# Optimization experiments

Hardware: AMD Instinct MI355X
Metric: run time of the kernel (lower is better)

The kernel has to match this reference:

```python
import jax, jax.numpy as jnp
import numpy as np

N_ITER = 3

def setup_inputs() -> dict:
    key = jax.random.key(0)
    k1, k2 = jax.random.split(key)
    x = jax.random.normal(k1, (8, 1024, 512), dtype=jnp.float32)
    W = jax.random.normal(k2, (4, 512, 512), dtype=jnp.float32)
    return {"x": x, "W": W}

def reference(x, W):
    # x: [B, N, D], W: [H, D, D]
    B, N, D = x.shape
    H = W.shape[0]
    scale = D ** (-0.5)
    logits = jnp.zeros((B, H, N, N), dtype=x.dtype)
    rw = None
    for _ in range(N_ITER):
        rw = jax.nn.softmax(logits, axis=-1)              # [B, H, N, N]
        # per-head bilinear scores: (x @ W_h) @ x^T * scale, batched over heads
        logits = jnp.einsum('bnd,hde,bme->bhnm', x, W, x) * scale
    # routing_weights @ x, then mean over heads -> [B, N, D]
    out = jnp.einsum('bhnm,bmd->bhnd', rw, x)
    return jnp.mean(out, axis=1)
```

## Files before the change

kernel.cpp:

```cpp
#include <hip/hip_runtime.h>
#include <math.h>

#define B_ 8
#define N_ 1024
#define D_ 512
#define H_ 4
#define ND (N_ * D_)
#define DD (D_ * D_)
#define NN (N_ * N_)

typedef _Float16 f16;
typedef f16 f16x8 __attribute__((ext_vector_type(8)));
typedef float f32x4 __attribute__((ext_vector_type(4)));

typedef __attribute__((address_space(3))) void lds_void;
typedef __attribute__((address_space(1))) void g_void;


#define MFMA8(QR, QC, AV, BV, IB)                                             \
    _Pragma("unroll")                                                         \
    for (int i_ = 0; i_ < 2; ++i_) {                                          \
        const int ii_ = (IB) + i_;                                            \
        _Pragma("unroll")                                                     \
        for (int j_ = 0; j_ < 2; ++j_) {                                      \
            acc[(QR)*4+ii_][(QC)*2+j_] = __builtin_amdgcn_mfma_f32_16x16x32_f16(AV[ii_][0], BV[j_][0], acc[(QR)*4+ii_][(QC)*2+j_], 0, 0, 0); \
            acc[(QR)*4+ii_][(QC)*2+j_] = __builtin_amdgcn_mfma_f32_16x16x32_f16(AV[ii_][1], BV[j_][1], acc[(QR)*4+ii_][(QC)*2+j_], 0, 0, 0); \
        }                                                                     \
    }

#define READ_A(AV, PA, HALF)                                                  \
    _Pragma("unroll")                                                         \
    for (int i_ = 0; i_ < 4; ++i_) {                                          \
        const int ra_ = (HALF) * 128 + wr * 64 + i_ * 16 + fr;                \
        AV[i_][0] = *(const f16x8*)(PA + ra_ * 64 + sw0 * 8);                 \
        AV[i_][1] = *(const f16x8*)(PA + ra_ * 64 + sw1 * 8);                 \
    }

#define READ_B(BV, PB, HALF)                                                  \
    _Pragma("unroll")                                                         \
    for (int j_ = 0; j_ < 2; ++j_) {                                          \
        const int rb_ = (HALF) * 128 + wc * 32 + j_ * 16 + fr;                \
        BV[j_][0] = *(const f16x8*)(PB + rb_ * 64 + sw0 * 8);                 \
        BV[j_][1] = *(const f16x8*)(PB + rb_ * 64 + sw1 * 8);                 \
    }

#define PHASE_RA(QR, QC, AV, BV, READS, STAGE, TAIL)                          \
    __builtin_amdgcn_s_barrier();                                             \
    asm volatile("s_waitcnt lgkmcnt(0)" ::: "memory");                        \
    __builtin_amdgcn_sched_barrier(0);                                        \
    __builtin_amdgcn_s_setprio(1);                                            \
    MFMA8(QR, QC, AV, BV, 0);                                                 \
    __builtin_amdgcn_s_setprio(0);                                            \
    __builtin_amdgcn_sched_barrier(0);                                        \
    READS;                                                                    \
    __builtin_amdgcn_sched_barrier(0);                                        \
    STAGE;                                                                    \
    __builtin_amdgcn_s_setprio(1);                                            \
    MFMA8(QR, QC, AV, BV, 2);                                                 \
    __builtin_amdgcn_s_setprio(0);                                            \
    TAIL;

template<int LDA, int LDB, int LDC, int KTOT>
__device__ __forceinline__ void gemm256(
    const f16* __restrict__ A, const f16* __restrict__ B,
    f16* __restrict__ C, float scale, int m0, int n0)
{
    constexpr int NT = KTOT / 64;
    static_assert(NT >= 2 && (NT % 2) == 0, "NT must be even");
    __shared__ f16 sA0[256 * 64];
    __shared__ f16 sB0[256 * 64];
    __shared__ f16 sA1[256 * 64];
    __shared__ f16 sB1[256 * 64];

    const int t = threadIdx.x;
    const int w = t >> 6, l = t & 63;
    const int fr = l & 15, fq = l >> 4;
    const int wr = w >> 2, wc = w & 3;
    const int lr = l >> 3, lc = l & 7;
    const int swc = lc ^ lr;
    const int sw0 = fq ^ (fr & 7);
    const int sw1 = (4 + fq) ^ (fr & 7);

    f32x4 acc[8][4] = {};

    auto stageA = [&](f16* buf, int half, int kt) {
#pragma unroll
        for (int i = 0; i < 2; ++i) {
            const int r0 = half * 128 + i * 64 + w * 8;
            const f16* g = A + (size_t)(m0 + r0 + lr) * LDA + kt * 64 + swc * 8;
            __builtin_amdgcn_global_load_lds((g_void*)g, (lds_void*)(buf + r0 * 64), 16, 0, 0);
        }
    };
    auto stageB = [&](f16* buf, int half, int kt) {
#pragma unroll
        for (int i = 0; i < 2; ++i) {
            const int r0 = half * 128 + i * 64 + w * 8;
            const f16* g = B + (size_t)(n0 + r0 + lr) * LDB + kt * 64 + swc * 8;
            __builtin_amdgcn_global_load_lds((g_void*)g, (lds_void*)(buf + r0 * 64), 16, 0, 0);
        }
    };

    stageA(sA0, 0, 0); stageB(sB0, 0, 0);
    stageA(sA0, 1, 0); stageB(sB0, 1, 0);
    stageA(sA1, 0, 1); stageB(sB1, 0, 1);
    asm volatile("s_waitcnt vmcnt(4)" ::: "memory");
    __builtin_amdgcn_s_barrier();

    f16x8 X[4][2], Y[4][2], U[2][2], V[2][2];
    READ_A(X, sA0, 0);
    READ_B(U, sB0, 0);

#define TAILCNT(KT)                                                           \
    { if ((KT) + 2 < NT) { asm volatile("s_waitcnt vmcnt(4)" ::: "memory"); } \
      else               { asm volatile("s_waitcnt vmcnt(0)" ::: "memory"); } }

#pragma unroll
    for (int tt = 0; tt < NT / 2; ++tt) {
        const int te = 2 * tt, to = 2 * tt + 1;
        PHASE_RA(0, 0, X, U, { READ_B(V, sB0, 1); },
                 { if (te + 1 < NT) stageA(sA1, 1, te + 1); }, {});
        PHASE_RA(0, 1, X, V, { READ_A(Y, sA0, 1); },
                 { if (te + 1 < NT) stageB(sB1, 1, te + 1); }, {});
        PHASE_RA(1, 1, Y, V, {},
                 { if (te + 2 < NT) stageA(sA0, 0, te + 2); }, {});
        PHASE_RA(1, 0, Y, U,
                 { if (te + 1 < NT) { READ_A(X, sA1, 0); READ_B(V, sB1, 0); } },
                 { if (te + 2 < NT) stageB(sB0, 0, te + 2); }, TAILCNT(te));
        PHASE_RA(0, 0, X, V, { READ_B(U, sB1, 1); },
                 { if (to + 1 < NT) stageA(sA0, 1, to + 1); }, {});
        PHASE_RA(0, 1, X, U, { READ_A(Y, sA1, 1); },
                 { if (to + 1 < NT) stageB(sB0, 1, to + 1); }, {});
        PHASE_RA(1, 1, Y, U, {},
                 { if (to + 2 < NT) stageA(sA1, 0, to + 2); }, {});
        PHASE_RA(1, 0, Y, V,
                 { if (to + 1 < NT) { READ_A(X, sA0, 0); READ_B(U, sB0, 0); } },
                 { if (to + 2 < NT) stageB(sB1, 0, to + 2); }, TAILCNT(to));
    }
#undef TAILCNT

#pragma unroll
    for (int ri = 0; ri < 8; ++ri)
#pragma unroll
        for (int cj = 0; cj < 4; ++cj)
#pragma unroll
            for (int rr = 0; rr < 4; ++rr) {
                const int row = m0 + (ri >> 2) * 128 + wr * 64 + (ri & 3) * 16 + fq * 4 + rr;
                const int col = n0 + (cj >> 1) * 128 + wc * 32 + (cj & 1) * 16 + fr;
                C[(size_t)row * LDC + col] = (f16)(acc[ri][cj][rr] * scale);
            }
}

template<int LDA, int LDB, int LDC, int KTOT>
__device__ __forceinline__ void single_core_f32(
    const f16* __restrict__ A, const f16* __restrict__ B0,
    float* __restrict__ C, int n0, int c0)
{
    __shared__ f16 sA[128 * 32];
    __shared__ f16 sB0[128 * 32];

    const int t = threadIdx.x;
    const int w = t >> 6;
    const int l = t & 63;
    const int lrow = l >> 2;
    const int lch  = l & 3;
    const int wr = w >> 1, wc = w & 1;
    const int fr = l & 15;
    const int fq = l >> 4;

    f32x4 acc[4][4] = {};

    for (int k0 = 0; k0 < KTOT; k0 += 32) {
#pragma unroll
        for (int i = 0; i < 2; ++i) {
            const int rb  = w * 2 + i;
            const int row = rb * 16 + lrow;
            const f16* ga = A + (size_t)(n0 + row) * LDA + k0 + lch * 8;
            __builtin_amdgcn_global_load_lds((g_void*)ga, (lds_void*)(sA + rb * 512), 16, 0, 0);
            const f16* gb0 = B0 + (size_t)(c0 + row) * LDB + k0 + lch * 8;
            __builtin_amdgcn_global_load_lds((g_void*)gb0, (lds_void*)(sB0 + rb * 512), 16, 0, 0);
        }
        __syncthreads();

        f16x8 a[4], b0[4];
#pragma unroll
        for (int i = 0; i < 4; ++i) {
            a[i]  = *(const f16x8*)(sA  + (wr * 64 + i * 16 + fr) * 32 + fq * 8);
            b0[i] = *(const f16x8*)(sB0 + (wc * 64 + i * 16 + fr) * 32 + fq * 8);
        }

#pragma unroll
        for (int i = 0; i < 4; ++i)
#pragma unroll
            for (int j = 0; j < 4; ++j)
                acc[i][j] = __builtin_amdgcn_mfma_f32_16x16x32_f16(a[i], b0[j], acc[i][j], 0, 0, 0);
        __syncthreads();
    }

#pragma unroll
    for (int i = 0; i < 4; ++i)
#pragma unroll
        for (int j = 0; j < 4; ++j)
#pragma unroll
            for (int r = 0; r < 4; ++r) {
                const int row = n0 + wr * 64 + i * 16 + fq * 4 + r;
                const int col = c0 + wc * 64 + j * 16 + fr;
                C[(size_t)row * LDC + col] = acc[i][j][r];
            }
}

__global__ __launch_bounds__(512, 2) void k_g1(
    const f16* __restrict__ xfh, const f16* __restrict__ wTh,
    f16* __restrict__ Yh)
{
    const int i = blockIdx.x;
    const int b = i & 7;
    const int li = i >> 3;
    const int h = li >> 3;
    const int tile = li & 7;
    const int m0 = (tile >> 1) * 256;
    const int n0 = (tile & 1) * 256;
    const int z = b * 4 + h;
    gemm256<D_, D_, D_, D_>(
        xfh + (size_t)b * ND,
        wTh + (size_t)h * DD,
        Yh + (size_t)z * ND, 1.0f, m0, n0);
}

__global__ __launch_bounds__(512, 2) void k_g2(
    const f16* __restrict__ Yh, const f16* __restrict__ xfh,
    f16* __restrict__ S)
{
    const int i = blockIdx.x;
    const int b = i & 7;
    const int li = i >> 3;
    const int h = li >> 4;
    const int tile = li & 15;
    const int m0 = (tile >> 2) * 256;
    const int n0 = (tile & 3) * 256;
    const int z = b * 4 + h;
    gemm256<D_, D_, N_, D_>(
        Yh + (size_t)z * ND,
        xfh + (size_t)b * ND,
        S + (size_t)z * NN, 0.044194173824159216f, m0, n0);
}

__global__ __launch_bounds__(256) void softmax_mean(
    const f16* __restrict__ S, f16* __restrict__ Pb)
{
    const int wave = threadIdx.x >> 6;
    const int l = threadIdx.x & 63;
    const int i = blockIdx.x;
    const int b = i & 7;
    const int rg = i >> 3;
    const int row = rg * 4 + wave;

    float o[16];
#pragma unroll
    for (int k = 0; k < 16; ++k) o[k] = 0.f;

#pragma unroll
    for (int h = 0; h < 4; ++h) {
        const f16x8* p = (const f16x8*)(S + ((size_t)(b * 4 + h) * N_ + row) * N_);
        f16x8 v0 = p[l * 2], v1 = p[l * 2 + 1];
        float f[16];
#pragma unroll
        for (int k = 0; k < 8; ++k) { f[k] = (float)v0[k]; f[k + 8] = (float)v1[k]; }
        float m = f[0];
#pragma unroll
        for (int k = 1; k < 16; ++k) m = fmaxf(m, f[k]);
#pragma unroll
        for (int off = 32; off > 0; off >>= 1) m = fmaxf(m, __shfl_xor(m, off));
        float s = 0.f;
#pragma unroll
        for (int k = 0; k < 16; ++k) { f[k] = __expf(f[k] - m); s += f[k]; }
#pragma unroll
        for (int off = 32; off > 0; off >>= 1) s += __shfl_xor(s, off);
        const float q = 0.25f / s;
#pragma unroll
        for (int k = 0; k < 16; ++k) o[k] += f[k] * q;
    }

    f16x8 o0, o1;
#pragma unroll
    for (int k = 0; k < 8; ++k) { o0[k] = (f16)o[k]; o1[k] = (f16)o[k + 8]; }
    f16x8* qp = (f16x8*)(Pb + ((size_t)b * N_ + row) * N_);
    qp[l * 2] = o0;
    qp[l * 2 + 1] = o1;
}

__global__ __launch_bounds__(256, 2) void k_g4b(
    const f16* __restrict__ Pb, const f16* __restrict__ xT,
    float* __restrict__ out)
{
    const int i = blockIdx.x;
    const int b = i & 7;
    const int li = i >> 3;
    const int m0 = (li >> 2) * 128;
    const int d0 = (li & 3) * 128;
    single_core_f32<N_, N_, D_, N_>(
        Pb + (size_t)b * NN,
        xT + (size_t)b * ND,
        out + (size_t)b * ND, m0, d0);
}

__global__ __launch_bounds__(256) void decomp_xw(
    const float* __restrict__ x, const float* __restrict__ W,
    f16* __restrict__ xfh, f16* __restrict__ xT, f16* __restrict__ wTh)
{
    __shared__ f16 tile[64][65];
    __shared__ float tw[64][65];
    const int t = threadIdx.x;
    const int z = blockIdx.z;
    if (z < 8) {
        const int b = z, n0 = blockIdx.y * 64, d0 = blockIdx.x * 64;
        const float* xb = x + (size_t)b * ND;
#pragma unroll
        for (int p = 0; p < 16; ++p) {
            const int idx = t + p * 256;
            const int r = idx >> 6, c = idx & 63;
            const float v = xb[(size_t)(n0 + r) * D_ + d0 + c];
            const f16 h = (f16)v;
            xfh[(size_t)b * ND + (size_t)(n0 + r) * D_ + d0 + c] = h;
            tile[r][c] = h;
        }
        __syncthreads();
#pragma unroll
        for (int p = 0; p < 16; ++p) {
            const int idx = t + p * 256;
            const int r = idx >> 6, c = idx & 63;
            xT[(size_t)b * ND + (size_t)(d0 + r) * N_ + n0 + c] = tile[c][r];
        }
    } else {
        if (blockIdx.y >= 8) return;
        const int h = z - 8, d0 = blockIdx.y * 64, e0 = blockIdx.x * 64;
        const float* Wh = W + (size_t)h * DD;
#pragma unroll
        for (int p = 0; p < 16; ++p) {
            const int idx = t + p * 256;
            const int r = idx >> 6, c = idx & 63;
            tw[r][c] = Wh[(size_t)(d0 + r) * D_ + e0 + c];
        }
        __syncthreads();
#pragma unroll
        for (int p = 0; p < 16; ++p) {
            const int idx = t + p * 256;
            const int r = idx >> 6, c = idx & 63;
            wTh[(size_t)h * DD + (size_t)(e0 + r) * D_ + d0 + c] = (f16)tw[c][r];
        }
    }
}

extern "C" void kernel_launch(void* const* d_in, const int* in_sizes, int n_in,
                              void* d_out, int out_size, void* d_ws, size_t ws_size,
                              hipStream_t stream) {
    const float* x = (const float*)d_in[0];
    const float* W = (const float*)d_in[1];
    float* out = (float*)d_out;

    char* ws = (char*)d_ws;
    const size_t MB = 1024 * 1024;
    f16*   xfh = (f16*)(ws + 0 * MB);
    f16*   xT  = (f16*)(ws + 8 * MB);
    f16*   wTh = (f16*)(ws + 16 * MB);
    f16*   Yh  = (f16*)(ws + 20 * MB);
    f16*   S   = (f16*)(ws + 52 * MB);
    f16*   Pb  = (f16*)(ws + 116 * MB);

    decomp_xw<<<dim3(8, 16, 12), 256, 0, stream>>>(x, W, xfh, xT, wTh);

    k_g1<<<dim3(256), 512, 0, stream>>>(xfh, wTh, Yh);
    k_g2<<<dim3(512), 512, 0, stream>>>(Yh, xfh, S);
    softmax_mean<<<dim3(2048), 256, 0, stream>>>(S, Pb);
    k_g4b<<<dim3(256), 256, 0, stream>>>(Pb, xT, out);
}
```

Before: 169.6 us.

## Vectorize transpose kernel, batch softmax loads, split score GEMM launch

```diff
diff --git a/kernel.cpp b/kernel.cpp
--- a/kernel.cpp
+++ b/kernel.cpp
@@ -10,6 +10,7 @@
 #define NN (N_ * N_)
 
 typedef _Float16 f16;
+typedef f16 f16x4 __attribute__((ext_vector_type(4)));
 typedef f16 f16x8 __attribute__((ext_vector_type(8)));
 typedef float f32x4 __attribute__((ext_vector_type(4)));
 
@@ -228,11 +229,11 @@
 
 __global__ __launch_bounds__(512, 2) void k_g2(
     const f16* __restrict__ Yh, const f16* __restrict__ xfh,
-    f16* __restrict__ S)
+    f16* __restrict__ S, int libase)
 {
     const int i = blockIdx.x;
     const int b = i & 7;
-    const int li = i >> 3;
+    const int li = (i >> 3) + libase * 32;
     const int h = li >> 4;
     const int tile = li & 15;
     const int m0 = (tile >> 2) * 256;
@@ -254,17 +255,23 @@
     const int rg = i >> 3;
     const int row = rg * 4 + wave;
 
-    float o[16];
-#pragma unroll
-    for (int k = 0; k < 16; ++k) o[k] = 0.f;
-
+    f16x8 va[4][2];
 #pragma unroll
     for (int h = 0; h < 4; ++h) {
         const f16x8* p = (const f16x8*)(S + ((size_t)(b * 4 + h) * N_ + row) * N_);
-        f16x8 v0 = p[l * 2], v1 = p[l * 2 + 1];
+        va[h][0] = p[l * 2];
+        va[h][1] = p[l * 2 + 1];
+    }
+
+    float o[16];
+#pragma unroll
+    for (int k = 0; k < 16; ++k) o[k] = 0.f;
+
+#pragma unroll
+    for (int h = 0; h < 4; ++h) {
         float f[16];
 #pragma unroll
-        for (int k = 0; k < 8; ++k) { f[k] = (float)v0[k]; f[k + 8] = (float)v1[k]; }
+        for (int k = 0; k < 8; ++k) { f[k] = (float)va[h][0][k]; f[k + 8] = (float)va[h][1][k]; }
         float m = f[0];
 #pragma unroll
         for (int k = 1; k < 16; ++k) m = fmaxf(m, f[k]);
@@ -307,45 +314,53 @@
     const float* __restrict__ x, const float* __restrict__ W,
     f16* __restrict__ xfh, f16* __restrict__ xT, f16* __restrict__ wTh)
 {
-    __shared__ f16 tile[64][65];
-    __shared__ float tw[64][65];
+    __shared__ f16 tile[64][68];
+    __shared__ float tw[64][68];
     const int t = threadIdx.x;
     const int z = blockIdx.z;
     if (z < 8) {
         const int b = z, n0 = blockIdx.y * 64, d0 = blockIdx.x * 64;
         const float* xb = x + (size_t)b * ND;
 #pragma unroll
-        for (int p = 0; p < 16; ++p) {
-            const int idx = t + p * 256;
-            const int r = idx >> 6, c = idx & 63;
-            const float v = xb[(size_t)(n0 + r) * D_ + d0 + c];
-            const f16 h = (f16)v;
-            xfh[(size_t)b * ND + (size_t)(n0 + r) * D_ + d0 + c] = h;
-            tile[r][c] = h;
+        for (int p = 0; p < 4; ++p) {
+            const int vid = t + p * 256;
+            const int r = vid >> 4, c4 = vid & 15;
+            const float4 v = *(const float4*)(xb + (size_t)(n0 + r) * D_ + d0 + c4 * 4);
+            f16x4 hv;
+            hv[0] = (f16)v.x; hv[1] = (f16)v.y; hv[2] = (f16)v.z; hv[3] = (f16)v.w;
+            *(f16x4*)(xfh + (size_t)b * ND + (size_t)(n0 + r) * D_ + d0 + c4 * 4) = hv;
+            *(f16x4*)(&tile[r][c4 * 4]) = hv;
         }
         __syncthreads();
 #pragma unroll
-        for (int p = 0; p < 16; ++p) {
-            const int idx = t + p * 256;
-            const int r = idx >> 6, c = idx & 63;
-            xT[(size_t)b * ND + (size_t)(d0 + r) * N_ + n0 + c] = tile[c][r];
+        for (int p = 0; p < 4; ++p) {
+            const int vid = t + p * 256;
+            const int r = vid >> 4, c4 = vid & 15;
+            f16x4 hv;
+#pragma unroll
+            for (int j = 0; j < 4; ++j) hv[j] = tile[c4 * 4 + j][r];
+            *(f16x4*)(xT + (size_t)b * ND + (size_t)(d0 + r) * N_ + n0 + c4 * 4) = hv;
         }
     } else {
         if (blockIdx.y >= 8) return;
         const int h = z - 8, d0 = blockIdx.y * 64, e0 = blockIdx.x * 64;
         const float* Wh = W + (size_t)h * DD;
 #pragma unroll
-        for (int p = 0; p < 16; ++p) {
-            const int idx = t + p * 256;
-            const int r = idx >> 6, c = idx & 63;
-            tw[r][c] = Wh[(size_t)(d0 + r) * D_ + e0 + c];
+        for (int p = 0; p < 4; ++p) {
+            const int vid = t + p * 256;
+            const int r = vid >> 4, c4 = vid & 15;
+            const float4 v = *(const float4*)(Wh + (size_t)(d0 + r) * D_ + e0 + c4 * 4);
+            *(float4*)(&tw[r][c4 * 4]) = v;
         }
         __syncthreads();
 #pragma unroll
-        for (int p = 0; p < 16; ++p) {
-            const int idx = t + p * 256;
-            const int r = idx >> 6, c = idx & 63;
-            wTh[(size_t)h * DD + (size_t)(e0 + r) * D_ + d0 + c] = (f16)tw[c][r];
+        for (int p = 0; p < 4; ++p) {
+            const int vid = t + p * 256;
+            const int r = vid >> 4, c4 = vid & 15;
+            f16x4 hv;
+#pragma unroll
+            for (int j = 0; j < 4; ++j) hv[j] = (f16)tw[c4 * 4 + j][r];
+            *(f16x4*)(wTh + (size_t)h * DD + (size_t)(e0 + r) * D_ + d0 + c4 * 4) = hv;
         }
     }
 }
@@ -369,7 +384,8 @@
     decomp_xw<<<dim3(8, 16, 12), 256, 0, stream>>>(x, W, xfh, xT, wTh);
 
     k_g1<<<dim3(256), 512, 0, stream>>>(xfh, wTh, Yh);
-    k_g2<<<dim3(512), 512, 0, stream>>>(Yh, xfh, S);
+    k_g2<<<dim3(256), 512, 0, stream>>>(Yh, xfh, S, 0);
+    k_g2<<<dim3(256), 512, 0, stream>>>(Yh, xfh, S, 1);
     softmax_mean<<<dim3(2048), 256, 0, stream>>>(S, Pb);
     k_g4b<<<dim3(256), 256, 0, stream>>>(Pb, xT, out);
 }
```

Measured after the change: 173.0 us. 1.02x slower.
